# Kernel tuning notes

Measured on AMD Instinct MI355X. Metric: run time of the kernel, lower is better.

The kernel has to match this reference:

```python
import jax, jax.numpy as jnp
import numpy as np

N_HEADS = 8


def setup_inputs() -> dict:
    key = jax.random.key(0)
    k1, k2 = jax.random.split(key)
    image_qkv = jax.random.normal(k1, (2, 1536, 4096), dtype=jnp.float32)
    st_qkv = jax.random.normal(k2, (2, 1536, 1024), dtype=jnp.float32)
    return {"image_qkv": image_qkv, "st_qkv": st_qkv}


def reference(image_qkv, st_qkv):
    bs, width, img_len = image_qkv.shape
    st_len = st_qkv.shape[2]
    assert width % (3 * N_HEADS) == 0
    ch = width // (3 * N_HEADS)
    hc = N_HEADS * ch

    img_q, img_k, img_v = (image_qkv[:, i * hc:(i + 1) * hc] for i in range(3))
    st_q, st_k, st_v = (st_qkv[:, i * hc:(i + 1) * hc] for i in range(3))

    scale = 1.0 / jnp.sqrt(jnp.sqrt(jnp.float32(ch)))

    def split_heads(x, length):  # [bs, H*ch, L] -> [bs*H, ch, L]
        return x.reshape(bs * N_HEADS, ch, length)

    # image queries attend over st keys/values (softmax applied)
    w_i = jnp.einsum('bct,bcs->bts', split_heads(img_q, img_len) * scale,
                     split_heads(st_k, st_len) * scale)
    w_i = jax.nn.softmax(w_i.astype(jnp.float32), axis=-1).astype(w_i.dtype)
    attn_i = jnp.einsum('bts,bcs->bct', w_i, split_heads(st_v, st_len)).reshape(bs, -1, img_len)

    # st queries attend over image keys/values (NOTE: original code has NO softmax here)
    w_st = jnp.einsum('bct,bcs->bts', split_heads(st_q, st_len) * scale,
                      split_heads(img_k, img_len) * scale)
    attn_st = jnp.einsum('bts,bcs->bct', w_st, split_heads(img_v, img_len)).reshape(bs, -1, st_len)

    return attn_i, attn_st
```

## Files before the change

kernel.cpp:

```cpp
#include <hip/hip_runtime.h>
#include <hip/hip_bf16.h>
#include <stdint.h>

#define DEVI __device__ __forceinline__

typedef __attribute__((ext_vector_type(8))) short short8;
typedef __attribute__((ext_vector_type(16))) float f32x16;
typedef __attribute__((ext_vector_type(4))) float f32x4;
typedef __attribute__((ext_vector_type(2))) unsigned int uint2v;
typedef unsigned short ushortT;

union U8 { short8 s8; unsigned u[4]; };

DEVI unsigned short f2bf(float f) {
  unsigned u = __builtin_bit_cast(unsigned, f);
  u += 0x7fffu + ((u >> 16) & 1u);
  return (unsigned short)(u >> 16);
}
DEVI unsigned pk2(float lo, float hi) {
  return (unsigned)f2bf(lo) | ((unsigned)f2bf(hi) << 16);
}
DEVI unsigned cvtpk(float lo, float hi) {
  unsigned r;
  asm("v_cvt_pk_bf16_f32 %0, %1, %2" : "=v"(r) : "v"(lo), "v"(hi));
  return r;
}
DEVI float exp2a(float x) { return __builtin_amdgcn_exp2f(x); }

#define MFMA32 __builtin_amdgcn_mfma_f32_32x32x16_bf16
#define C_L2E 0.18033688011112042f

__global__ __launch_bounds__(256) void prep_kernel(
    const float* __restrict__ st, ushortT* __restrict__ kfp,
    ushortT* __restrict__ vfp) {
  const int bid = blockIdx.x;
  const int bh = bid >> 4, t = bid & 15;
  const int b = bh >> 3, h = bh & 7;
  const float* kbase = st + ((size_t)(b * 1536 + 512 + h * 64)) * 1024;
  const float* vbase = st + ((size_t)(b * 1536 + 1024 + h * 64)) * 1024;
  ushortT* ko = kfp + ((size_t)bh * 16 + t) * 4096;
  ushortT* vo = vfp + ((size_t)bh * 16 + t) * 4096;
  const int tid = threadIdx.x;

  __shared__ float kf[64][65];
  {
    const int c = tid >> 2, s16 = (tid & 3) * 16;
    const float* kp = kbase + (size_t)c * 1024 + t * 64 + s16;
    f32x4 a = *(const f32x4*)kp, b4 = *(const f32x4*)(kp + 4),
          c4 = *(const f32x4*)(kp + 8), d4 = *(const f32x4*)(kp + 12);
#pragma unroll
    for (int j = 0; j < 4; ++j) {
      kf[c][s16 + j] = a[j];
      kf[c][s16 + 4 + j] = b4[j];
      kf[c][s16 + 8 + j] = c4[j];
      kf[c][s16 + 12 + j] = d4[j];
    }
  }
#pragma unroll
  for (int rep = 0; rep < 2; ++rep) {
    const int pair = tid + rep * 256;
    const int c = pair >> 3, oct = pair & 7;
    const float* vp = vbase + (size_t)c * 1024 + t * 64 + oct * 8;
    f32x4 lo = *(const f32x4*)vp, hp = *(const f32x4*)(vp + 4);
    uint2v la, ha;
    la[0] = pk2(lo[0], lo[1]); la[1] = pk2(lo[2], lo[3]);
    ha[0] = pk2(hp[0], hp[1]); ha[1] = pk2(hp[2], hp[3]);
    const int ci = c >> 5, ln = c & 31;
    const int ss = oct >> 2, kk2 = (oct >> 1) & 1, o1 = oct & 1;
    const int f = ss * 4 + kk2 * 2 + ci;
    *(uint2v*)(vo + ((size_t)f * 64 + ln) * 8 + o1 * 4) = la;
    *(uint2v*)(vo + ((size_t)f * 64 + 32 + ln) * 8 + o1 * 4) = ha;
  }
  __syncthreads();
  {
    const int lane = tid & 63, kk = tid >> 6;
    const int hi = lane >> 5, ln = lane & 31;
#pragma unroll
    for (int half = 0; half < 2; ++half) {
      float v8[8];
#pragma unroll
      for (int j = 0; j < 8; ++j) v8[j] = kf[kk * 16 + hi * 8 + j][half * 32 + ln];
      U8 u;
#pragma unroll
      for (int i = 0; i < 4; ++i) u.u[i] = pk2(v8[2 * i], v8[2 * i + 1]);
      *(short8*)(ko + ((size_t)(half * 4 + kk) * 64 + lane) * 8) = u.s8;
    }
  }
}

DEVI void stage_tile(ushortT (*lds)[2][16][512], int buf,
                     const ushortT* kf_half, const ushortT* vf_half,
                     int wsh, int fpbase, int lane, int tile) {
#pragma unroll
  for (int j = 0; j < 4; ++j) {
    const int fp = fpbase + j;
    const ushortT* src =
        (fp < 8 ? kf_half + (size_t)tile * 4096 + (size_t)fp * 512
                : vf_half + (size_t)tile * 4096 + (size_t)(fp - 8) * 512) +
        lane * 8;
    __builtin_amdgcn_global_load_lds(
        (const __attribute__((address_space(1))) void*)src,
        (__attribute__((address_space(3))) void*)&lds[buf][wsh][fp][0], 16, 0, 0);
  }
}

__global__ __launch_bounds__(512, 3) void fused_kernel(
    const float* __restrict__ img, const ushortT* __restrict__ kfp,
    const ushortT* __restrict__ vfp, float* __restrict__ out0,
    float* __restrict__ Mws) {
  __shared__ __align__(16) char pool[65536];
  const int tid = threadIdx.x;
  const int bid = blockIdx.x;
  const int w = tid >> 6, lane = tid & 63, hi = lane >> 5, ln = lane & 31;

  if (bid < 512) {
    const int bh = bid >> 5, tb = bid & 31;
    const int b = bh >> 3, h = bh & 7;
    const float* qbase = img + ((size_t)(b * 1536 + h * 64)) * 4096;
    float* obase = out0 + ((size_t)(b * 512 + h * 64)) * 4096;

    const int wt = w & 3, wsh = w >> 2;
    const int fpbase = wt * 4;
    const int tcol = tb * 128 + wt * 32 + ln;

    ushortT (*lds)[2][16][512] = (ushortT (*)[2][16][512])pool;
    const ushortT* kf_half = kfp + ((size_t)bh * 16 + wsh * 8) * 4096;
    const ushortT* vf_half = vfp + ((size_t)bh * 16 + wsh * 8) * 4096;

    stage_tile(lds, 0, kf_half, vf_half, wsh, fpbase, lane, 0);

    short8 qf[4];
#pragma unroll
    for (int k = 0; k < 4; ++k) {
      const float* qp = qbase + (size_t)(k * 16 + hi * 8) * 4096 + tcol;
      float q8[8];
#pragma unroll
      for (int j = 0; j < 8; ++j) q8[j] = qp[(size_t)j * 4096] * C_L2E;
      U8 u;
#pragma unroll
      for (int i = 0; i < 4; ++i) u.u[i] = pk2(q8[2 * i], q8[2 * i + 1]);
      qf[k] = u.s8;
    }

    f32x16 o0 = {}, o1 = {};
    float la0 = 0.f, la1 = 0.f, la2 = 0.f, la3 = 0.f;

    __syncthreads();

    for (int i = 0; i < 8; ++i) {
      const int cur = i & 1;
      const ushortT(*L)[512] = lds[cur][wsh];

      f32x16 sc0 = {}, sc1 = {};
      {
        short8 kfr[8];
#pragma unroll
        for (int f = 0; f < 8; ++f) kfr[f] = *(const short8*)&L[f][lane * 8];
        __builtin_amdgcn_s_setprio(1);
        sc0 = MFMA32(kfr[0], qf[0], sc0, 0, 0, 0);
        sc1 = MFMA32(kfr[4], qf[0], sc1, 0, 0, 0);
        sc0 = MFMA32(kfr[1], qf[1], sc0, 0, 0, 0);
        sc1 = MFMA32(kfr[5], qf[1], sc1, 0, 0, 0);
        sc0 = MFMA32(kfr[2], qf[2], sc0, 0, 0, 0);
        sc1 = MFMA32(kfr[6], qf[2], sc1, 0, 0, 0);
        sc0 = MFMA32(kfr[3], qf[3], sc0, 0, 0, 0);
        sc1 = MFMA32(kfr[7], qf[3], sc1, 0, 0, 0);
        __builtin_amdgcn_s_setprio(0);
      }

      if (i + 1 < 8)
        stage_tile(lds, cur ^ 1, kf_half, vf_half, wsh, fpbase, lane, i + 1);

#pragma unroll
      for (int q = 0; q < 16; q += 4) {
        float p0 = exp2a(sc0[q]);
        float p1 = exp2a(sc0[q + 1]);
        float p2 = exp2a(sc0[q + 2]);
        float p3 = exp2a(sc0[q + 3]);
        sc0[q] = p0; sc0[q + 1] = p1; sc0[q + 2] = p2; sc0[q + 3] = p3;
        la0 += p0; la1 += p1; la2 += p2; la3 += p3;
      }
#pragma unroll
      for (int q = 0; q < 16; q += 4) {
        float p0 = exp2a(sc1[q]);
        float p1 = exp2a(sc1[q + 1]);
        float p2 = exp2a(sc1[q + 2]);
        float p3 = exp2a(sc1[q + 3]);
        sc1[q] = p0; sc1[q + 1] = p1; sc1[q + 2] = p2; sc1[q + 3] = p3;
        la0 += p0; la1 += p1; la2 += p2; la3 += p3;
      }

#pragma unroll
      for (int ss = 0; ss < 2; ++ss) {
        const f32x16& sc = ss ? sc1 : sc0;
        U8 B0, B1;
        B0.u[0] = cvtpk(sc[0], sc[1]);   B0.u[1] = cvtpk(sc[2], sc[3]);
        B0.u[2] = cvtpk(sc[4], sc[5]);   B0.u[3] = cvtpk(sc[6], sc[7]);
        B1.u[0] = cvtpk(sc[8], sc[9]);   B1.u[1] = cvtpk(sc[10], sc[11]);
        B1.u[2] = cvtpk(sc[12], sc[13]); B1.u[3] = cvtpk(sc[14], sc[15]);
        short8 v00 = *(const short8*)&L[8 + ss * 4 + 0][lane * 8];
        short8 v01 = *(const short8*)&L[8 + ss * 4 + 1][lane * 8];
        short8 v10 = *(const short8*)&L[8 + ss * 4 + 2][lane * 8];
        short8 v11 = *(const short8*)&L[8 + ss * 4 + 3][lane * 8];
        __builtin_amdgcn_s_setprio(1);
        o0 = MFMA32(v00, B0.s8, o0, 0, 0, 0);
        o1 = MFMA32(v01, B0.s8, o1, 0, 0, 0);
        o0 = MFMA32(v10, B1.s8, o0, 0, 0, 0);
        o1 = MFMA32(v11, B1.s8, o1, 0, 0, 0);
        __builtin_amdgcn_s_setprio(0);
      }
      __syncthreads();
    }

    float l = (la0 + la1) + (la2 + la3);
    l += __shfl_xor(l, 32);

    float (*mrg)[64][33] = (float (*)[64][33])pool;
    if (wsh == 1) {
#pragma unroll
      for (int q = 0; q < 16; ++q) {
        mrg[wt][lane][q] = o0[q];
        mrg[wt][lane][16 + q] = o1[q];
      }
      mrg[wt][lane][32] = l;
    }
    __syncthreads();
    if (wsh == 0) {
      const float linv = 1.0f / (l + mrg[wt][lane][32]);
#pragma unroll
      for (int q = 0; q < 16; ++q) {
        const int c = (q & 3) + 8 * (q >> 2) + 4 * hi;
        obase[(size_t)c * 4096 + tcol] = (o0[q] + mrg[wt][lane][q]) * linv;
        obase[(size_t)(c + 32) * 4096 + tcol] = (o1[q] + mrg[wt][lane][16 + q]) * linv;
      }
    }
  } else {
    const int gb = bid - 512;
    const int bh = gb >> 3, chunk = gb & 7;
    const int b = bh >> 3, h = bh & 7;
    const float* kbase = img + ((size_t)(b * 1536 + 512 + h * 64)) * 4096;
    const float* vbase = img + ((size_t)(b * 1536 + 1024 + h * 64)) * 4096;

    f32x16 m00 = {}, m01 = {}, m10 = {}, m11 = {};
    const int sbeg = chunk * 512 + w * 64;
    for (int s0 = sbeg; s0 < sbeg + 64; s0 += 16) {
      const int sa = s0 + hi * 8;
      short8 av[2], bk[2];
#pragma unroll
      for (int ci = 0; ci < 2; ++ci) {
        const float* vp = vbase + (size_t)(ci * 32 + ln) * 4096 + sa;
        f32x4 lo = *(const f32x4*)vp, hp = *(const f32x4*)(vp + 4);
        U8 u;
        u.u[0] = pk2(lo[0], lo[1]); u.u[1] = pk2(lo[2], lo[3]);
        u.u[2] = pk2(hp[0], hp[1]); u.u[3] = pk2(hp[2], hp[3]);
        av[ci] = u.s8;
      }
#pragma unroll
      for (int cj = 0; cj < 2; ++cj) {
        const float* kp = kbase + (size_t)(cj * 32 + ln) * 4096 + sa;
        f32x4 lo = *(const f32x4*)kp, hp = *(const f32x4*)(kp + 4);
        U8 u;
        u.u[0] = pk2(lo[0], lo[1]); u.u[1] = pk2(lo[2], lo[3]);
        u.u[2] = pk2(hp[0], hp[1]); u.u[3] = pk2(hp[2], hp[3]);
        bk[cj] = u.s8;
      }
      m00 = MFMA32(av[0], bk[0], m00, 0, 0, 0);
      m01 = MFMA32(av[0], bk[1], m01, 0, 0, 0);
      m10 = MFMA32(av[1], bk[0], m10, 0, 0, 0);
      m11 = MFMA32(av[1], bk[1], m11, 0, 0, 0);
    }

    float (*part)[64][64] = (float (*)[64][64])pool;
    if (w < 4) {
#pragma unroll
      for (int q = 0; q < 16; ++q) {
        const int cr = (q & 3) + 8 * (q >> 2) + 4 * hi;
        part[w][cr][ln] = m00[q];
        part[w][cr][32 + ln] = m01[q];
        part[w][32 + cr][ln] = m10[q];
        part[w][32 + cr][32 + ln] = m11[q];
      }
    }
    __syncthreads();
    if (w >= 4) {
      const int pw = w - 4;
#pragma unroll
      for (int q = 0; q < 16; ++q) {
        const int cr = (q & 3) + 8 * (q >> 2) + 4 * hi;
        part[pw][cr][ln] += m00[q];
        part[pw][cr][32 + ln] += m01[q];
        part[pw][32 + cr][ln] += m10[q];
        part[pw][32 + cr][32 + ln] += m11[q];
      }
    }
    __syncthreads();
#pragma unroll
    for (int i = 0; i < 8; ++i) {
      const int e = tid + i * 512;
      const int c = e >> 6, cp = e & 63;
      Mws[(size_t)gb * 4096 + c * 64 + cp] =
          (part[0][c][cp] + part[1][c][cp] + part[2][c][cp] + part[3][c][cp]) *
          0.125f;
    }
  }
}

__global__ __launch_bounds__(256) void attn_st2_kernel(
    const float* __restrict__ st, const float* __restrict__ Mws,
    float* __restrict__ out1) {
  const int tid = threadIdx.x;
  const int bh = blockIdx.x >> 2;
  const int tt = blockIdx.x & 3;
  const int b = bh >> 3, h = bh & 7;
  const float* qbase = st + ((size_t)(b * 1536 + h * 64)) * 1024;
  float* o1 = out1 + ((size_t)(b * 512 + h * 64)) * 1024;

  __shared__ float Ms[64][64];
  char* msb = (char*)&Ms[0][0];

#pragma unroll
  for (int i = 0; i < 16; ++i) {
    const int e = tid + i * 256;
    const int c = e >> 6, cp = e & 63;
    const float* mp = Mws + (size_t)bh * 8 * 4096 + c * 64 + cp;
    float s = 0.f;
#pragma unroll
    for (int ch = 0; ch < 8; ++ch) s += mp[(size_t)ch * 4096];
    *(float*)(msb + c * 256 + ((cp * 4) ^ ((c & 7) << 5))) = s;
  }
  __syncthreads();

  const int w = tid >> 6, lane = tid & 63, hi = lane >> 5, ln = lane & 31;

  short8 aM0[4], aM1[4];
#pragma unroll
  for (int k = 0; k < 4; ++k) {
#pragma unroll
    for (int ci = 0; ci < 2; ++ci) {
      const int row = ci * 32 + ln;
      const int bo = k * 64 + hi * 32;
      const char* rp = msb + row * 256;
      const int swz = (row & 7) << 5;
      f32x4 lo = *(const f32x4*)(rp + (bo ^ swz));
      f32x4 hp = *(const f32x4*)(rp + ((bo + 16) ^ swz));
      U8 u;
      u.u[0] = pk2(lo[0], lo[1]); u.u[1] = pk2(lo[2], lo[3]);
      u.u[2] = pk2(hp[0], hp[1]); u.u[3] = pk2(hp[2], hp[3]);
      if (ci) aM1[k] = u.s8; else aM0[k] = u.s8;
    }
  }

#pragma unroll
  for (int nt = 0; nt < 2; ++nt) {
    const int t = tt * 256 + w * 64 + nt * 32 + ln;
    short8 bq[4];
#pragma unroll
    for (int k = 0; k < 4; ++k) {
      const float* qp = qbase + (size_t)(k * 16 + hi * 8) * 1024 + t;
      float q8[8];
#pragma unroll
      for (int j = 0; j < 8; ++j) q8[j] = qp[(size_t)j * 1024];
      U8 u;
#pragma unroll
      for (int i = 0; i < 4; ++i) u.u[i] = pk2(q8[2 * i], q8[2 * i + 1]);
      bq[k] = u.s8;
    }
    f32x16 a0 = {}, a1 = {};
#pragma unroll
    for (int k = 0; k < 4; ++k) {
      a0 = MFMA32(aM0[k], bq[k], a0, 0, 0, 0);
      a1 = MFMA32(aM1[k], bq[k], a1, 0, 0, 0);
    }
#pragma unroll
    for (int q = 0; q < 16; ++q) {
      const int cr = (q & 3) + 8 * (q >> 2) + 4 * hi;
      o1[(size_t)cr * 1024 + t] = a0[q];
      o1[(size_t)(cr + 32) * 1024 + t] = a1[q];
    }
  }
}

extern "C" void kernel_launch(void* const* d_in, const int* in_sizes, int n_in,
                              void* d_out, int out_size, void* d_ws, size_t ws_size,
                              hipStream_t stream) {
  const float* img = (const float*)d_in[0];
  const float* st = (const float*)d_in[1];
  float* out0 = (float*)d_out;
  float* out1 = out0 + (size_t)2 * 512 * 4096;
  char* ws = (char*)d_ws;
  const size_t MB = 1u << 20;

  ushortT* kfp;
  ushortT* vfp;
  float* Ms;
  if (ws_size >= 6 * MB) {
    kfp = (ushortT*)ws; vfp = (ushortT*)(ws + 2 * MB); Ms = (float*)(ws + 4 * MB);
  } else {
    kfp = (ushortT*)out1; vfp = (ushortT*)((char*)out1 + 2 * MB);
    Ms = (float*)ws;
  }

  hipLaunchKernelGGL(prep_kernel, dim3(256), dim3(256), 0, stream, st, kfp, vfp);
  hipLaunchKernelGGL(fused_kernel, dim3(640), dim3(512), 0, stream, img, kfp, vfp,
                     out0, Ms);
  hipLaunchKernelGGL(attn_st2_kernel, dim3(64), dim3(256), 0, stream, st, Ms, out1);
}
```

Baseline: 48.84 us.

## Restructure kernel schedule: merge prep with M-reduction, fuse st2 into attention kernel

The K/V bf16 prep and the image K·V^T reduction (M) now run together in one aux kernel. The st2 output blocks are appended to the main attention kernel's grid, cutting one launch and overlapping that work with attention. The attention kernel moves from 512-thread blocks that split the key range across two wave halves to 256-thread blocks that walk all 16 tiles themselves. This drops the cross-half LDS merge and one sync per block. In exchange, the serial loop per block is longer and the M reduction now uses 4 waves each covering twice as many rows.

```diff
diff --git a/kernel.cpp b/kernel.cpp
--- a/kernel.cpp
+++ b/kernel.cpp
@@ -30,220 +30,76 @@
 #define MFMA32 __builtin_amdgcn_mfma_f32_32x32x16_bf16
 #define C_L2E 0.18033688011112042f
 
-__global__ __launch_bounds__(256) void prep_kernel(
-    const float* __restrict__ st, ushortT* __restrict__ kfp,
-    ushortT* __restrict__ vfp) {
-  const int bid = blockIdx.x;
-  const int bh = bid >> 4, t = bid & 15;
-  const int b = bh >> 3, h = bh & 7;
-  const float* kbase = st + ((size_t)(b * 1536 + 512 + h * 64)) * 1024;
-  const float* vbase = st + ((size_t)(b * 1536 + 1024 + h * 64)) * 1024;
-  ushortT* ko = kfp + ((size_t)bh * 16 + t) * 4096;
-  ushortT* vo = vfp + ((size_t)bh * 16 + t) * 4096;
-  const int tid = threadIdx.x;
-
-  __shared__ float kf[64][65];
-  {
-    const int c = tid >> 2, s16 = (tid & 3) * 16;
-    const float* kp = kbase + (size_t)c * 1024 + t * 64 + s16;
-    f32x4 a = *(const f32x4*)kp, b4 = *(const f32x4*)(kp + 4),
-          c4 = *(const f32x4*)(kp + 8), d4 = *(const f32x4*)(kp + 12);
-#pragma unroll
-    for (int j = 0; j < 4; ++j) {
-      kf[c][s16 + j] = a[j];
-      kf[c][s16 + 4 + j] = b4[j];
-      kf[c][s16 + 8 + j] = c4[j];
-      kf[c][s16 + 12 + j] = d4[j];
-    }
-  }
-#pragma unroll
-  for (int rep = 0; rep < 2; ++rep) {
-    const int pair = tid + rep * 256;
-    const int c = pair >> 3, oct = pair & 7;
-    const float* vp = vbase + (size_t)c * 1024 + t * 64 + oct * 8;
-    f32x4 lo = *(const f32x4*)vp, hp = *(const f32x4*)(vp + 4);
-    uint2v la, ha;
-    la[0] = pk2(lo[0], lo[1]); la[1] = pk2(lo[2], lo[3]);
-    ha[0] = pk2(hp[0], hp[1]); ha[1] = pk2(hp[2], hp[3]);
-    const int ci = c >> 5, ln = c & 31;
-    const int ss = oct >> 2, kk2 = (oct >> 1) & 1, o1 = oct & 1;
-    const int f = ss * 4 + kk2 * 2 + ci;
-    *(uint2v*)(vo + ((size_t)f * 64 + ln) * 8 + o1 * 4) = la;
-    *(uint2v*)(vo + ((size_t)f * 64 + 32 + ln) * 8 + o1 * 4) = ha;
-  }
-  __syncthreads();
-  {
-    const int lane = tid & 63, kk = tid >> 6;
-    const int hi = lane >> 5, ln = lane & 31;
-#pragma unroll
-    for (int half = 0; half < 2; ++half) {
-      float v8[8];
-#pragma unroll
-      for (int j = 0; j < 8; ++j) v8[j] = kf[kk * 16 + hi * 8 + j][half * 32 + ln];
-      U8 u;
-#pragma unroll
-      for (int i = 0; i < 4; ++i) u.u[i] = pk2(v8[2 * i], v8[2 * i + 1]);
-      *(short8*)(ko + ((size_t)(half * 4 + kk) * 64 + lane) * 8) = u.s8;
-    }
-  }
-}
-
-DEVI void stage_tile(ushortT (*lds)[2][16][512], int buf,
-                     const ushortT* kf_half, const ushortT* vf_half,
-                     int wsh, int fpbase, int lane, int tile) {
-#pragma unroll
-  for (int j = 0; j < 4; ++j) {
-    const int fp = fpbase + j;
-    const ushortT* src =
-        (fp < 8 ? kf_half + (size_t)tile * 4096 + (size_t)fp * 512
-                : vf_half + (size_t)tile * 4096 + (size_t)(fp - 8) * 512) +
-        lane * 8;
-    __builtin_amdgcn_global_load_lds(
-        (const __attribute__((address_space(1))) void*)src,
-        (__attribute__((address_space(3))) void*)&lds[buf][wsh][fp][0], 16, 0, 0);
-  }
-}
-
-__global__ __launch_bounds__(512, 3) void fused_kernel(
-    const float* __restrict__ img, const ushortT* __restrict__ kfp,
-    const ushortT* __restrict__ vfp, float* __restrict__ out0,
+__global__ __launch_bounds__(256) void aux_kernel(
+    const float* __restrict__ img, const float* __restrict__ st,
+    ushortT* __restrict__ kfp, ushortT* __restrict__ vfp,
     float* __restrict__ Mws) {
-  __shared__ __align__(16) char pool[65536];
+  __shared__ __align__(16) char pool[32768];
   const int tid = threadIdx.x;
   const int bid = blockIdx.x;
   const int w = tid >> 6, lane = tid & 63, hi = lane >> 5, ln = lane & 31;
 
-  if (bid < 512) {
-    const int bh = bid >> 5, tb = bid & 31;
+  if (bid < 256) {
+    const int bh = bid >> 4, t = bid & 15;
     const int b = bh >> 3, h = bh & 7;
-    const float* qbase = img + ((size_t)(b * 1536 + h * 64)) * 4096;
-    float* obase = out0 + ((size_t)(b * 512 + h * 64)) * 4096;
-
-    const int wt = w & 3, wsh = w >> 2;
-    const int fpbase = wt * 4;
-    const int tcol = tb * 128 + wt * 32 + ln;
-
-    ushortT (*lds)[2][16][512] = (ushortT (*)[2][16][512])pool;
-    const ushortT* kf_half = kfp + ((size_t)bh * 16 + wsh * 8) * 4096;
-    const ushortT* vf_half = vfp + ((size_t)bh * 16 + wsh * 8) * 4096;
-
-    stage_tile(lds, 0, kf_half, vf_half, wsh, fpbase, lane, 0);
-
-    short8 qf[4];
-#pragma unroll
-    for (int k = 0; k < 4; ++k) {
-      const float* qp = qbase + (size_t)(k * 16 + hi * 8) * 4096 + tcol;
-      float q8[8];
-#pragma unroll
-      for (int j = 0; j < 8; ++j) q8[j] = qp[(size_t)j * 4096] * C_L2E;
-      U8 u;
-#pragma unroll
-      for (int i = 0; i < 4; ++i) u.u[i] = pk2(q8[2 * i], q8[2 * i + 1]);
-      qf[k] = u.s8;
-    }
-
-    f32x16 o0 = {}, o1 = {};
-    float la0 = 0.f, la1 = 0.f, la2 = 0.f, la3 = 0.f;
-
+    const float* kbase = st + ((size_t)(b * 1536 + 512 + h * 64)) * 1024;
+    const float* vbase = st + ((size_t)(b * 1536 + 1024 + h * 64)) * 1024;
+    ushortT* ko = kfp + ((size_t)bh * 16 + t) * 4096;
+    ushortT* vo = vfp + ((size_t)bh * 16 + t) * 4096;
+
+    float (*kf)[65] = (float (*)[65])pool;
+    {
+      const int c = tid >> 2, s16 = (tid & 3) * 16;
+      const float* kp = kbase + (size_t)c * 1024 + t * 64 + s16;
+      f32x4 a = *(const f32x4*)kp, b4 = *(const f32x4*)(kp + 4),
+            c4 = *(const f32x4*)(kp + 8), d4 = *(const f32x4*)(kp + 12);
+#pragma unroll
+      for (int j = 0; j < 4; ++j) {
+        kf[c][s16 + j] = a[j];
+        kf[c][s16 + 4 + j] = b4[j];
+        kf[c][s16 + 8 + j] = c4[j];
+        kf[c][s16 + 12 + j] = d4[j];
+      }
+    }
+#pragma unroll
+    for (int rep = 0; rep < 2; ++rep) {
+      const int pair = tid + rep * 256;
+      const int c = pair >> 3, oct = pair & 7;
+      const float* vp = vbase + (size_t)c * 1024 + t * 64 + oct * 8;
+      f32x4 lo = *(const f32x4*)vp, hp = *(const f32x4*)(vp + 4);
+      uint2v la, ha;
+      la[0] = pk2(lo[0], lo[1]); la[1] = pk2(lo[2], lo[3]);
+      ha[0] = pk2(hp[0], hp[1]); ha[1] = pk2(hp[2], hp[3]);
+      const int ci = c >> 5, lnn = c & 31;
+      const int ss = oct >> 2, kk2 = (oct >> 1) & 1, o1 = oct & 1;
+      const int f = ss * 4 + kk2 * 2 + ci;
+      *(uint2v*)(vo + ((size_t)f * 64 + lnn) * 8 + o1 * 4) = la;
+      *(uint2v*)(vo + ((size_t)f * 64 + 32 + lnn) * 8 + o1 * 4) = ha;
+    }
     __syncthreads();
-
-    for (int i = 0; i < 8; ++i) {
-      const int cur = i & 1;
-      const ushortT(*L)[512] = lds[cur][wsh];
-
-      f32x16 sc0 = {}, sc1 = {};
-      {
-        short8 kfr[8];
-#pragma unroll
-        for (int f = 0; f < 8; ++f) kfr[f] = *(const short8*)&L[f][lane * 8];
-        __builtin_amdgcn_s_setprio(1);
-        sc0 = MFMA32(kfr[0], qf[0], sc0, 0, 0, 0);
-        sc1 = MFMA32(kfr[4], qf[0], sc1, 0, 0, 0);
-        sc0 = MFMA32(kfr[1], qf[1], sc0, 0, 0, 0);
-        sc1 = MFMA32(kfr[5], qf[1], sc1, 0, 0, 0);
-        sc0 = MFMA32(kfr[2], qf[2], sc0, 0, 0, 0);
-        sc1 = MFMA32(kfr[6], qf[2], sc1, 0, 0, 0);
-        sc0 = MFMA32(kfr[3], qf[3], sc0, 0, 0, 0);
-        sc1 = MFMA32(kfr[7], qf[3], sc1, 0, 0, 0);
-        __builtin_amdgcn_s_setprio(0);
-      }
-
-      if (i + 1 < 8)
-        stage_tile(lds, cur ^ 1, kf_half, vf_half, wsh, fpbase, lane, i + 1);
-
-#pragma unroll
-      for (int q = 0; q < 16; q += 4) {
-        float p0 = exp2a(sc0[q]);
-        float p1 = exp2a(sc0[q + 1]);
-        float p2 = exp2a(sc0[q + 2]);
-        float p3 = exp2a(sc0[q + 3]);
-        sc0[q] = p0; sc0[q + 1] = p1; sc0[q + 2] = p2; sc0[q + 3] = p3;
-        la0 += p0; la1 += p1; la2 += p2; la3 += p3;
-      }
-#pragma unroll
-      for (int q = 0; q < 16; q += 4) {
-        float p0 = exp2a(sc1[q]);
-        float p1 = exp2a(sc1[q + 1]);
-        float p2 = exp2a(sc1[q + 2]);
-        float p3 = exp2a(sc1[q + 3]);
-        sc1[q] = p0; sc1[q + 1] = p1; sc1[q + 2] = p2; sc1[q + 3] = p3;
-        la0 += p0; la1 += p1; la2 += p2; la3 += p3;
-      }
-
-#pragma unroll
-      for (int ss = 0; ss < 2; ++ss) {
-        const f32x16& sc = ss ? sc1 : sc0;
-        U8 B0, B1;
-        B0.u[0] = cvtpk(sc[0], sc[1]);   B0.u[1] = cvtpk(sc[2], sc[3]);
-        B0.u[2] = cvtpk(sc[4], sc[5]);   B0.u[3] = cvtpk(sc[6], sc[7]);
-        B1.u[0] = cvtpk(sc[8], sc[9]);   B1.u[1] = cvtpk(sc[10], sc[11]);
-        B1.u[2] = cvtpk(sc[12], sc[13]); B1.u[3] = cvtpk(sc[14], sc[15]);
-        short8 v00 = *(const short8*)&L[8 + ss * 4 + 0][lane * 8];
-        short8 v01 = *(const short8*)&L[8 + ss * 4 + 1][lane * 8];
-        short8 v10 = *(const short8*)&L[8 + ss * 4 + 2][lane * 8];
-        short8 v11 = *(const short8*)&L[8 + ss * 4 + 3][lane * 8];
-        __builtin_amdgcn_s_setprio(1);
-        o0 = MFMA32(v00, B0.s8, o0, 0, 0, 0);
-        o1 = MFMA32(v01, B0.s8, o1, 0, 0, 0);
-        o0 = MFMA32(v10, B1.s8, o0, 0, 0, 0);
-        o1 = MFMA32(v11, B1.s8, o1, 0, 0, 0);
-        __builtin_amdgcn_s_setprio(0);
-      }
-      __syncthreads();
-    }
-
-    float l = (la0 + la1) + (la2 + la3);
-    l += __shfl_xor(l, 32);
-
-    float (*mrg)[64][33] = (float (*)[64][33])pool;
-    if (wsh == 1) {
-#pragma unroll
-      for (int q = 0; q < 16; ++q) {
-        mrg[wt][lane][q] = o0[q];
-        mrg[wt][lane][16 + q] = o1[q];
-      }
-      mrg[wt][lane][32] = l;
-    }
-    __syncthreads();
-    if (wsh == 0) {
-      const float linv = 1.0f / (l + mrg[wt][lane][32]);
-#pragma unroll
-      for (int q = 0; q < 16; ++q) {
-        const int c = (q & 3) + 8 * (q >> 2) + 4 * hi;
-        obase[(size_t)c * 4096 + tcol] = (o0[q] + mrg[wt][lane][q]) * linv;
-        obase[(size_t)(c + 32) * 4096 + tcol] = (o1[q] + mrg[wt][lane][16 + q]) * linv;
+    {
+      const int kk = w;
+#pragma unroll
+      for (int half = 0; half < 2; ++half) {
+        float v8[8];
+#pragma unroll
+        for (int j = 0; j < 8; ++j) v8[j] = kf[kk * 16 + hi * 8 + j][half * 32 + ln];
+        U8 u;
+#pragma unroll
+        for (int i = 0; i < 4; ++i) u.u[i] = pk2(v8[2 * i], v8[2 * i + 1]);
+        *(short8*)(ko + ((size_t)(half * 4 + kk) * 64 + lane) * 8) = u.s8;
       }
     }
   } else {
-    const int gb = bid - 512;
+    const int gb = bid - 256;
     const int bh = gb >> 3, chunk = gb & 7;
     const int b = bh >> 3, h = bh & 7;
     const float* kbase = img + ((size_t)(b * 1536 + 512 + h * 64)) * 4096;
     const float* vbase = img + ((size_t)(b * 1536 + 1024 + h * 64)) * 4096;
 
     f32x16 m00 = {}, m01 = {}, m10 = {}, m11 = {};
-    const int sbeg = chunk * 512 + w * 64;
-    for (int s0 = sbeg; s0 < sbeg + 64; s0 += 16) {
+    const int sbeg = chunk * 512 + w * 128;
+    for (int s0 = sbeg; s0 < sbeg + 128; s0 += 16) {
       const int sa = s0 + hi * 8;
       short8 av[2], bk[2];
 #pragma unroll
@@ -271,7 +127,7 @@
     }
 
     float (*part)[64][64] = (float (*)[64][64])pool;
-    if (w < 4) {
+    if (w < 2) {
 #pragma unroll
       for (int q = 0; q < 16; ++q) {
         const int cr = (q & 3) + 8 * (q >> 2) + 4 * hi;
@@ -282,8 +138,8 @@
       }
     }
     __syncthreads();
-    if (w >= 4) {
-      const int pw = w - 4;
+    if (w >= 2) {
+      const int pw = w - 2;
 #pragma unroll
       for (int q = 0; q < 16; ++q) {
         const int cr = (q & 3) + 8 * (q >> 2) + 4 * hi;
@@ -295,28 +151,37 @@
     }
     __syncthreads();
 #pragma unroll
-    for (int i = 0; i < 8; ++i) {
-      const int e = tid + i * 512;
+    for (int i = 0; i < 16; ++i) {
+      const int e = tid + i * 256;
       const int c = e >> 6, cp = e & 63;
       Mws[(size_t)gb * 4096 + c * 64 + cp] =
-          (part[0][c][cp] + part[1][c][cp] + part[2][c][cp] + part[3][c][cp]) *
-          0.125f;
-    }
-  }
-}
-
-__global__ __launch_bounds__(256) void attn_st2_kernel(
-    const float* __restrict__ st, const float* __restrict__ Mws,
-    float* __restrict__ out1) {
-  const int tid = threadIdx.x;
-  const int bh = blockIdx.x >> 2;
-  const int tt = blockIdx.x & 3;
+          (part[0][c][cp] + part[1][c][cp]) * 0.125f;
+    }
+  }
+}
+
+DEVI void stage_tile(ushortT (*lds)[16][512], int buf, const ushortT* kf_all,
+                     const ushortT* vf_all, int fpbase, int lane, int tile) {
+#pragma unroll
+  for (int j = 0; j < 4; ++j) {
+    const int fp = fpbase + j;
+    const ushortT* src =
+        (fp < 8 ? kf_all + (size_t)tile * 4096 + (size_t)fp * 512
+                : vf_all + (size_t)tile * 4096 + (size_t)(fp - 8) * 512) +
+        lane * 8;
+    __builtin_amdgcn_global_load_lds(
+        (const __attribute__((address_space(1))) void*)src,
+        (__attribute__((address_space(3))) void*)&lds[buf][fp][0], 16, 0, 0);
+  }
+}
+
+DEVI void st2_body(const float* __restrict__ st, const float* __restrict__ Mws,
+                   float* __restrict__ out1, int sb, int tid, char* pool) {
+  const int bh = sb >> 2, tt = sb & 3;
   const int b = bh >> 3, h = bh & 7;
   const float* qbase = st + ((size_t)(b * 1536 + h * 64)) * 1024;
   float* o1 = out1 + ((size_t)(b * 512 + h * 64)) * 1024;
-
-  __shared__ float Ms[64][64];
-  char* msb = (char*)&Ms[0][0];
+  char* msb = pool;
 
 #pragma unroll
   for (int i = 0; i < 16; ++i) {
@@ -380,6 +245,137 @@
   }
 }
 
+template <bool WITH_ST2>
+__global__ __launch_bounds__(256, 3) void main_kernel(
+    const float* __restrict__ img, const ushortT* __restrict__ kfp,
+    const ushortT* __restrict__ vfp, const float* __restrict__ st,
+    const float* __restrict__ Mws, float* __restrict__ out0,
+    float* __restrict__ out1) {
+  __shared__ __align__(16) char pool[32768];
+  const int tid = threadIdx.x;
+  const int bid = blockIdx.x;
+
+  if (WITH_ST2 && bid >= 512) {
+    st2_body(st, Mws, out1, bid - 512, tid, pool);
+    return;
+  }
+
+  const int w = tid >> 6, lane = tid & 63, hi = lane >> 5, ln = lane & 31;
+  const int bh = bid >> 5, tb = bid & 31;
+  const int b = bh >> 3, h = bh & 7;
+  const float* qbase = img + ((size_t)(b * 1536 + h * 64)) * 4096;
+  float* obase = out0 + ((size_t)(b * 512 + h * 64)) * 4096;
+
+  const int fpbase = w * 4;
+  const int tcol = tb * 128 + w * 32 + ln;
+
+  ushortT (*lds)[16][512] = (ushortT (*)[16][512])pool;
+  const ushortT* kf_all = kfp + (size_t)bh * 16 * 4096;
+  const ushortT* vf_all = vfp + (size_t)bh * 16 * 4096;
+
+  stage_tile(lds, 0, kf_all, vf_all, fpbase, lane, 0);
+
+  short8 qf[4];
+#pragma unroll
+  for (int k = 0; k < 4; ++k) {
+    const float* qp = qbase + (size_t)(k * 16 + hi * 8) * 4096 + tcol;
+    float q8[8];
+#pragma unroll
+    for (int j = 0; j < 8; ++j) q8[j] = qp[(size_t)j * 4096] * C_L2E;
+    U8 u;
+#pragma unroll
+    for (int i = 0; i < 4; ++i) u.u[i] = pk2(q8[2 * i], q8[2 * i + 1]);
+    qf[k] = u.s8;
+  }
+
+  f32x16 o0 = {}, o1 = {};
+  float la0 = 0.f, la1 = 0.f, la2 = 0.f, la3 = 0.f;
+
+  __syncthreads();
+
+  for (int i = 0; i < 16; ++i) {
+    const int cur = i & 1;
+    const ushortT(*L)[512] = lds[cur];
+
+    f32x16 sc0 = {}, sc1 = {};
+    {
+      short8 kfr[8];
+#pragma unroll
+      for (int f = 0; f < 8; ++f) kfr[f] = *(const short8*)&L[f][lane * 8];
+      __builtin_amdgcn_s_setprio(1);
+      sc0 = MFMA32(kfr[0], qf[0], sc0, 0, 0, 0);
+      sc1 = MFMA32(kfr[4], qf[0], sc1, 0, 0, 0);
+      sc0 = MFMA32(kfr[1], qf[1], sc0, 0, 0, 0);
+      sc1 = MFMA32(kfr[5], qf[1], sc1, 0, 0, 0);
+      sc0 = MFMA32(kfr[2], qf[2], sc0, 0, 0, 0);
+      sc1 = MFMA32(kfr[6], qf[2], sc1, 0, 0, 0);
+      sc0 = MFMA32(kfr[3], qf[3], sc0, 0, 0, 0);
+      sc1 = MFMA32(kfr[7], qf[3], sc1, 0, 0, 0);
+      __builtin_amdgcn_s_setprio(0);
+    }
+
+    if (i + 1 < 16)
+      stage_tile(lds, cur ^ 1, kf_all, vf_all, fpbase, lane, i + 1);
+
+#pragma unroll
+    for (int q = 0; q < 16; q += 4) {
+      float p0 = exp2a(sc0[q]);
+      float p1 = exp2a(sc0[q + 1]);
+      float p2 = exp2a(sc0[q + 2]);
+      float p3 = exp2a(sc0[q + 3]);
+      sc0[q] = p0; sc0[q + 1] = p1; sc0[q + 2] = p2; sc0[q + 3] = p3;
+      la0 += p0; la1 += p1; la2 += p2; la3 += p3;
+    }
+#pragma unroll
+    for (int q = 0; q < 16; q += 4) {
+      float p0 = exp2a(sc1[q]);
+      float p1 = exp2a(sc1[q + 1]);
+      float p2 = exp2a(sc1[q + 2]);
+      float p3 = exp2a(sc1[q + 3]);
+      sc1[q] = p0; sc1[q + 1] = p1; sc1[q + 2] = p2; sc1[q + 3] = p3;
+      la0 += p0; la1 += p1; la2 += p2; la3 += p3;
+    }
+
+#pragma unroll
+    for (int ss = 0; ss < 2; ++ss) {
+      const f32x16& sc = ss ? sc1 : sc0;
+      U8 B0, B1;
+      B0.u[0] = cvtpk(sc[0], sc[1]);   B0.u[1] = cvtpk(sc[2], sc[3]);
+      B0.u[2] = cvtpk(sc[4], sc[5]);   B0.u[3] = cvtpk(sc[6], sc[7]);
+      B1.u[0] = cvtpk(sc[8], sc[9]);   B1.u[1] = cvtpk(sc[10], sc[11]);
+      B1.u[2] = cvtpk(sc[12], sc[13]); B1.u[3] = cvtpk(sc[14], sc[15]);
+      short8 v00 = *(const short8*)&L[8 + ss * 4 + 0][lane * 8];
+      short8 v01 = *(const short8*)&L[8 + ss * 4 + 1][lane * 8];
+      short8 v10 = *(const short8*)&L[8 + ss * 4 + 2][lane * 8];
+      short8 v11 = *(const short8*)&L[8 + ss * 4 + 3][lane * 8];
+      __builtin_amdgcn_s_setprio(1);
+      o0 = MFMA32(v00, B0.s8, o0, 0, 0, 0);
+      o1 = MFMA32(v01, B0.s8, o1, 0, 0, 0);
+      o0 = MFMA32(v10, B1.s8, o0, 0, 0, 0);
+      o1 = MFMA32(v11, B1.s8, o1, 0, 0, 0);
+      __builtin_amdgcn_s_setprio(0);
+    }
+    if (i + 1 < 16) __syncthreads();
+  }
+
+  float l = (la0 + la1) + (la2 + la3);
+  l += __shfl_xor(l, 32);
+  const float linv = 1.0f / l;
+#pragma unroll
+  for (int q = 0; q < 16; ++q) {
+    const int c = (q & 3) + 8 * (q >> 2) + 4 * hi;
+    obase[(size_t)c * 4096 + tcol] = o0[q] * linv;
+    obase[(size_t)(c + 32) * 4096 + tcol] = o1[q] * linv;
+  }
+}
+
+__global__ __launch_bounds__(256) void st2_kernel(
+    const float* __restrict__ st, const float* __restrict__ Mws,
+    float* __restrict__ out1) {
+  __shared__ __align__(16) char pool[16384];
+  st2_body(st, Mws, out1, blockIdx.x, threadIdx.x, pool);
+}
+
 extern "C" void kernel_launch(void* const* d_in, const int* in_sizes, int n_in,
                               void* d_out, int out_size, void* d_ws, size_t ws_size,
                               hipStream_t stream) {
@@ -393,15 +389,22 @@
   ushortT* kfp;
   ushortT* vfp;
   float* Ms;
-  if (ws_size >= 6 * MB) {
+  bool fits = ws_size >= 6 * MB;
+  if (fits) {
     kfp = (ushortT*)ws; vfp = (ushortT*)(ws + 2 * MB); Ms = (float*)(ws + 4 * MB);
   } else {
     kfp = (ushortT*)out1; vfp = (ushortT*)((char*)out1 + 2 * MB);
     Ms = (float*)ws;
   }
 
-  hipLaunchKernelGGL(prep_kernel, dim3(256), dim3(256), 0, stream, st, kfp, vfp);
-  hipLaunchKernelGGL(fused_kernel, dim3(640), dim3(512), 0, stream, img, kfp, vfp,
-                     out0, Ms);
-  hipLaunchKernelGGL(attn_st2_kernel, dim3(64), dim3(256), 0, stream, st, Ms, out1);
-}
+  hipLaunchKernelGGL(aux_kernel, dim3(384), dim3(256), 0, stream, img, st, kfp,
+                     vfp, Ms);
+  if (fits) {
+    hipLaunchKernelGGL((main_kernel<true>), dim3(576), dim3(256), 0, stream, img,
+                       kfp, vfp, st, Ms, out0, out1);
+  } else {
+    hipLaunchKernelGGL((main_kernel<false>), dim3(512), dim3(256), 0, stream, img,
+                       kfp, vfp, st, Ms, out0, out1);
+    hipLaunchKernelGGL(st2_kernel, dim3(64), dim3(256), 0, stream, st, Ms, out1);
+  }
+}
```

Result: faster. 44.06 us (-9.8%).
